# Performance work log

Measured on AMD Instinct MI355X. Metric: run time of the kernel, lower is better.

## Reference

```python
import jax, jax.numpy as jnp
import numpy as np

C = 512
H_HEADS = 8
HEAD_DIM = C // H_HEADS


def setup_inputs() -> dict:
    key = jax.random.key(0)
    ks = jax.random.split(key, 6)
    B, Hs, Ws = 16, 32, 32
    x = jax.random.normal(ks[0], (B, C, Hs, Ws), dtype=jnp.float32)
    qkv_w = jax.random.normal(ks[1], (3 * C, C), dtype=jnp.float32) * 0.02
    proj_w = jax.random.normal(ks[2], (C, C), dtype=jnp.float32) * 0.02
    proj_b = jnp.zeros((C,), dtype=jnp.float32)
    ln_g = jnp.ones((C,), dtype=jnp.float32)
    ln_b = jnp.zeros((C,), dtype=jnp.float32)
    return {"x": x, "qkv_w": qkv_w, "proj_w": proj_w, "proj_b": proj_b,
            "ln_g": ln_g, "ln_b": ln_b}


def _layernorm(x, g, b, eps=1e-5):
    mu = jnp.mean(x, axis=-1, keepdims=True)
    var = jnp.var(x, axis=-1, keepdims=True)
    return (x - mu) * jax.lax.rsqrt(var + eps) * g + b


def reference(x, qkv_w, proj_w, proj_b, ln_g, ln_b):
    B, Cc, Hs, Ws = x.shape
    N = Hs * Ws
    # (B, N, C)
    x_flat = x.reshape(B, Cc, N).transpose(0, 2, 1)
    x_norm = _layernorm(x_flat, ln_g, ln_b)
    # qkv: torch Linear y = x @ W^T
    qkv = x_norm @ qkv_w.T  # (B, N, 3C)
    qkv = qkv.reshape(B, N, 3, H_HEADS, HEAD_DIM).transpose(2, 0, 3, 1, 4)
    q, k, v = qkv[0], qkv[1], qkv[2]  # (B, h, N, d)
    scale = HEAD_DIM ** -0.5
    attn = jnp.einsum('bhnd,bhmd->bhnm', q, k) * scale
    attn = jax.nn.softmax(attn, axis=-1)
    out = jnp.einsum('bhnm,bhmd->bhnd', attn, v)  # (B, h, N, d)
    out = out.transpose(0, 2, 1, 3).reshape(B, N, Cc)
    out = out @ proj_w.T + proj_b
    out = out + x_flat
    return out.transpose(0, 2, 1).reshape(B, Cc, Hs, Ws)
```

## Files before the change

### kernel.cpp

```cpp
#include <hip/hip_runtime.h>
#include <stdint.h>

typedef unsigned short u16;
typedef __attribute__((ext_vector_type(4))) float f32x4;
typedef __attribute__((ext_vector_type(8))) short s16x8;
typedef __attribute__((ext_vector_type(4))) unsigned short u16x4;
typedef __attribute__((ext_vector_type(8))) unsigned short u16x8;
typedef __attribute__((ext_vector_type(2))) unsigned int u32x2;

__device__ __forceinline__ u16 f2bf(float f) {
  union { float f; uint32_t u; } v; v.f = f;
  uint32_t r = (v.u + 0x7FFFu + ((v.u >> 16) & 1u)) >> 16;
  return (u16)r;
}

__device__ __forceinline__ void gload_lds16(const void* g, void* l) {
  __builtin_amdgcn_global_load_lds((const __attribute__((address_space(1))) uint32_t*)g,
                                   (__attribute__((address_space(3))) uint32_t*)l, 16, 0, 0);
}

__global__ __launch_bounds__(256) void cvt_kernel(const float* __restrict__ src,
                                                  u16* __restrict__ dst, int n) {
  const int i = (blockIdx.x * 256 + threadIdx.x) * 4;
  if (i < n) {
    f32x4 v = *(const f32x4*)(src + i);
    u16x4 p;
    p[0] = f2bf(v[0]); p[1] = f2bf(v[1]); p[2] = f2bf(v[2]); p[3] = f2bf(v[3]);
    *(u16x4*)(dst + i) = p;
  }
}

__global__ __launch_bounds__(256) void ln_kernel(const float* __restrict__ x,
                                                 const float* __restrict__ lng,
                                                 const float* __restrict__ lnb,
                                                 u16* __restrict__ xn) {
  __shared__ float xt[16][516];
  __shared__ float ps[16][16], pq[16][16];
  __shared__ float smu[16], srs[16];
  const int tid = threadIdx.x;
  const int tok0 = blockIdx.x << 4;
  const int b = tok0 >> 10;
  const int nb = tok0 & 1023;
  const float* xb = x + (size_t)b * 512 * 1024 + nb;
  {
    const int n4 = (tid & 3) * 4;
    const int cr = tid >> 2;
#pragma unroll
    for (int it = 0; it < 8; ++it) {
      const int c = it * 64 + cr;
      f32x4 v = *(const f32x4*)(xb + (size_t)c * 1024 + n4);
      xt[n4 + 0][c] = v[0]; xt[n4 + 1][c] = v[1];
      xt[n4 + 2][c] = v[2]; xt[n4 + 3][c] = v[3];
    }
  }
  __syncthreads();
  {
    const int n = tid & 15, part = tid >> 4;
    float s = 0.f, q = 0.f;
#pragma unroll
    for (int i = 0; i < 8; ++i) {
      f32x4 v = *(const f32x4*)&xt[n][part * 32 + i * 4];
#pragma unroll
      for (int j = 0; j < 4; ++j) { s += v[j]; q += v[j] * v[j]; }
    }
    ps[part][n] = s; pq[part][n] = q;
  }
  __syncthreads();
  if (tid < 16) {
    float s = 0.f, q = 0.f;
#pragma unroll
    for (int p = 0; p < 16; ++p) { s += ps[p][tid]; q += pq[p][tid]; }
    const float mu = s * (1.f / 512.f);
    const float var = q * (1.f / 512.f) - mu * mu;
    smu[tid] = mu; srs[tid] = rsqrtf(var + 1e-5f);
  }
  __syncthreads();
  {
    const int n = tid >> 4, sub = tid & 15;
    const float mu = smu[n], rs = srs[n];
    u16* dst = xn + (size_t)(tok0 + n) * 512;
#pragma unroll
    for (int i = 0; i < 4; ++i) {
      const int c = (sub + 16 * i) * 8;
      f32x4 v0 = *(const f32x4*)&xt[n][c];
      f32x4 v1 = *(const f32x4*)&xt[n][c + 4];
      f32x4 g0 = *(const f32x4*)(lng + c);
      f32x4 g1 = *(const f32x4*)(lng + c + 4);
      f32x4 b0 = *(const f32x4*)(lnb + c);
      f32x4 b1 = *(const f32x4*)(lnb + c + 4);
      u16x8 pk;
#pragma unroll
      for (int j = 0; j < 4; ++j) {
        pk[j]     = f2bf((v0[j] - mu) * rs * g0[j] + b0[j]);
        pk[4 + j] = f2bf((v1[j] - mu) * rs * g1[j] + b1[j]);
      }
      *(u16x8*)(dst + c) = pk;
    }
  }
}

template <int EPI>
__global__ __launch_bounds__(256) void gemm_bt(const u16* __restrict__ A,
                                               const u16* __restrict__ Bw,
                                               void* __restrict__ Cout,
                                               const float* __restrict__ bias,
                                               const float* __restrict__ resid,
                                               int M, int N, int K,
                                               long bsz, long csz, long rsz) {
  __shared__ u16 Al[128 * 32];
  __shared__ u16 Bl[128 * 32];
  const int tid = threadIdx.x;
  const int w = tid >> 6, lane = tid & 63;
  const int lg = lane >> 4, l15 = lane & 15;
  const int wr = w >> 1, wc = w & 1;
  const int m0 = blockIdx.x * 128, n0 = blockIdx.y * 128;
  const int z = blockIdx.z;
  const u16* Bz = Bw + (size_t)z * bsz;
  const float* Rz = (EPI == 1) ? resid + (size_t)z * rsz : nullptr;

  f32x4 acc[4][4];
#pragma unroll
  for (int i = 0; i < 4; ++i)
#pragma unroll
    for (int j = 0; j < 4; ++j) acc[i][j] = (f32x4){0.f, 0.f, 0.f, 0.f};

  const int sr = lane >> 2, sch = (lane & 3) * 8;
  for (int k0 = 0; k0 < K; k0 += 32) {
    __syncthreads();
#pragma unroll
    for (int i = 0; i < 2; ++i) {
      gload_lds16(A + (size_t)(m0 + w * 32 + i * 16 + sr) * K + k0 + sch,
                  &Al[(w * 32 + i * 16) * 32]);
      gload_lds16(Bz + (size_t)(n0 + w * 32 + i * 16 + sr) * K + k0 + sch,
                  &Bl[(w * 32 + i * 16) * 32]);
    }
    __syncthreads();
    s16x8 af[4], bfr[4];
#pragma unroll
    for (int mi = 0; mi < 4; ++mi)
      af[mi] = *(const s16x8*)&Al[(wr * 64 + mi * 16 + l15) * 32 + lg * 8];
#pragma unroll
    for (int ni = 0; ni < 4; ++ni)
      bfr[ni] = *(const s16x8*)&Bl[(wc * 64 + ni * 16 + l15) * 32 + lg * 8];
#pragma unroll
    for (int mi = 0; mi < 4; ++mi)
#pragma unroll
      for (int ni = 0; ni < 4; ++ni)
        acc[mi][ni] = __builtin_amdgcn_mfma_f32_16x16x32_bf16(af[mi], bfr[ni], acc[mi][ni], 0, 0, 0);
  }

  if (EPI == 0) {
    u16* C = (u16*)Cout;
#pragma unroll
    for (int mi = 0; mi < 4; ++mi)
#pragma unroll
      for (int ni = 0; ni < 4; ++ni) {
        const int col = n0 + wc * 64 + ni * 16 + l15;
#pragma unroll
        for (int r = 0; r < 4; ++r) {
          const int row = m0 + wr * 64 + mi * 16 + lg * 4 + r;
          C[(size_t)row * N + col] = f2bf(acc[mi][ni][r]);
        }
      }
  } else {
    float* C = (float*)Cout + (size_t)z * csz;
#pragma unroll
    for (int mi = 0; mi < 4; ++mi)
#pragma unroll
      for (int ni = 0; ni < 4; ++ni) {
        const int col = n0 + wc * 64 + ni * 16 + l15;
#pragma unroll
        for (int r = 0; r < 4; ++r) {
          const int row = m0 + wr * 64 + mi * 16 + lg * 4 + r;
          C[(size_t)row * N + col] = acc[mi][ni][r] + bias[row] + Rz[(size_t)row * N + col];
        }
      }
  }
}

__global__ __launch_bounds__(256) void attn_kernel(const u16* __restrict__ qkv,
                                                   u16* __restrict__ ao) {
  __shared__ union {
    struct { u16 K[64 * 64]; uint32_t Vt[64 * 34]; } s;
    struct { float O[4 * 32 * 68]; float ls[4 * 32]; } e;
  } sm;
  const int tid = threadIdx.x;
  const int w = tid >> 6, lane = tid & 63;
  const int lg = lane >> 4, l15 = lane & 15;
  const int qb = blockIdx.x & 7, bh = blockIdx.x >> 3;
  const int b = bh >> 3, h = bh & 7;
  const size_t base = (size_t)b * 1024 * 1536;
  const int qtok0 = qb * 128 + w * 32;

  s16x8 qf[2][2];
#pragma unroll
  for (int s = 0; s < 2; ++s)
#pragma unroll
    for (int qg = 0; qg < 2; ++qg)
      qf[s][qg] = *(const s16x8*)(qkv + base + (size_t)(qtok0 + qg * 16 + l15) * 1536 +
                                  h * 64 + lg * 8 + 32 * s);

  f32x4 o[2][4];
#pragma unroll
  for (int qg = 0; qg < 2; ++qg)
#pragma unroll
    for (int db = 0; db < 4; ++db) o[qg][db] = (f32x4){0.f, 0.f, 0.f, 0.f};
  float mrun[2] = {-1e30f, -1e30f};
  float lrun[2] = {0.f, 0.f};
  const float CE = 0.125f * 1.44269504f;

  for (int k0 = 0; k0 < 1024; k0 += 64) {
    __syncthreads();
    {
      const int r = lane >> 3, ch = lane & 7;
#pragma unroll
      for (int i = 0; i < 2; ++i) {
        const int row = w * 16 + i * 8 + r;
        const u16* src = qkv + base + (size_t)(k0 + row) * 1536 + 512 + h * 64 +
                         ((ch ^ (row & 7)) * 8);
        gload_lds16(src, &sm.s.K[(w * 16 + i * 8) * 64]);
      }
    }
    {
      const int kk = tid & 63, dc = tid >> 6;
      const u16* v0p = qkv + base + (size_t)(k0 + kk) * 1536 + 1024 + h * 64 + dc * 8;
      u16x8 va = *(const u16x8*)v0p;
      u16x8 vc = *(const u16x8*)(v0p + 32);
      u16* vt16 = (u16*)sm.s.Vt;
      const int kp2 = kk >> 1, klo = kk & 1;
#pragma unroll
      for (int i = 0; i < 8; ++i) {
        const int d0 = dc * 8 + i;
        vt16[(d0 * 34 + kp2) * 2 + klo] = va[i];
        vt16[((d0 + 32) * 34 + kp2) * 2 + klo] = vc[i];
      }
    }
    __syncthreads();

    f32x4 st[4][2];
#pragma unroll
    for (int kg = 0; kg < 4; ++kg)
#pragma unroll
      for (int qg = 0; qg < 2; ++qg) st[kg][qg] = (f32x4){0.f, 0.f, 0.f, 0.f};
#pragma unroll
    for (int s = 0; s < 2; ++s)
#pragma unroll
      for (int kg = 0; kg < 4; ++kg) {
        const int row = kg * 16 + l15;
        s16x8 kf = *(const s16x8*)&sm.s.K[row * 64 + ((lg * 8 + 32 * s) ^ ((row & 7) << 3))];
#pragma unroll
        for (int qg = 0; qg < 2; ++qg)
          st[kg][qg] = __builtin_amdgcn_mfma_f32_16x16x32_bf16(kf, qf[s][qg], st[kg][qg], 0, 0, 0);
      }

    float pvv[2][16];
#pragma unroll
    for (int qg = 0; qg < 2; ++qg) {
      float tmax = -1e30f;
#pragma unroll
      for (int kg = 0; kg < 4; ++kg)
#pragma unroll
        for (int r = 0; r < 4; ++r) tmax = fmaxf(tmax, st[kg][qg][r]);
      tmax = fmaxf(tmax, __shfl_xor(tmax, 16));
      tmax = fmaxf(tmax, __shfl_xor(tmax, 32));
      const float mnew = fmaxf(mrun[qg], tmax);
      const float corr = exp2f((mrun[qg] - mnew) * CE);
      mrun[qg] = mnew;
      float tsum = 0.f;
#pragma unroll
      for (int kg = 0; kg < 4; ++kg)
#pragma unroll
        for (int r = 0; r < 4; ++r) {
          const float p = exp2f((st[kg][qg][r] - mnew) * CE);
          pvv[qg][kg * 4 + r] = p;
          tsum += p;
        }
      tsum += __shfl_xor(tsum, 16);
      tsum += __shfl_xor(tsum, 32);
      lrun[qg] = lrun[qg] * corr + tsum;
#pragma unroll
      for (int db = 0; db < 4; ++db)
#pragma unroll
        for (int r = 0; r < 4; ++r) o[qg][db][r] *= corr;
    }

    s16x8 pa[2][2];
#pragma unroll
    for (int qg = 0; qg < 2; ++qg)
#pragma unroll
      for (int kh = 0; kh < 2; ++kh) {
        s16x8 f;
#pragma unroll
        for (int j = 0; j < 4; ++j) {
          f[j]     = (short)f2bf(pvv[qg][(2 * kh) * 4 + j]);
          f[4 + j] = (short)f2bf(pvv[qg][(2 * kh + 1) * 4 + j]);
        }
        pa[qg][kh] = f;
      }

#pragma unroll
    for (int kh = 0; kh < 2; ++kh)
#pragma unroll
      for (int db = 0; db < 4; ++db) {
        const int d = db * 16 + l15;
        const uint32_t* vtp = sm.s.Vt + d * 34;
        u32x2 va = *(const u32x2*)(vtp + 16 * kh + 2 * lg);
        u32x2 vb = *(const u32x2*)(vtp + 16 * kh + 8 + 2 * lg);
        s16x8 vf;
        vf[0] = (short)(va[0] & 0xffff); vf[1] = (short)(va[0] >> 16);
        vf[2] = (short)(va[1] & 0xffff); vf[3] = (short)(va[1] >> 16);
        vf[4] = (short)(vb[0] & 0xffff); vf[5] = (short)(vb[0] >> 16);
        vf[6] = (short)(vb[1] & 0xffff); vf[7] = (short)(vb[1] >> 16);
#pragma unroll
        for (int qg = 0; qg < 2; ++qg)
          o[qg][db] = __builtin_amdgcn_mfma_f32_16x16x32_bf16(pa[qg][kh], vf, o[qg][db], 0, 0, 0);
      }
  }

  __syncthreads();
  float* Ow = sm.e.O + w * 32 * 68;
#pragma unroll
  for (int qg = 0; qg < 2; ++qg)
#pragma unroll
    for (int db = 0; db < 4; ++db)
#pragma unroll
      for (int r = 0; r < 4; ++r)
        Ow[(qg * 16 + lg * 4 + r) * 68 + db * 16 + l15] = o[qg][db][r];
  if (lane < 16) {
    sm.e.ls[w * 32 + lane] = lrun[0];
    sm.e.ls[w * 32 + 16 + lane] = lrun[1];
  }
  __syncthreads();
  {
    const int q = lane & 31, dh = lane >> 5;
    const float inv = 1.0f / sm.e.ls[w * 32 + q];
    u16* dst = ao + (size_t)(b * 1024 + qtok0 + q) * 512 + h * 64 + dh * 32;
#pragma unroll
    for (int i = 0; i < 4; ++i) {
      f32x4 v0 = *(const f32x4*)&Ow[q * 68 + dh * 32 + i * 8];
      f32x4 v1 = *(const f32x4*)&Ow[q * 68 + dh * 32 + i * 8 + 4];
      u16x8 pk;
#pragma unroll
      for (int j = 0; j < 4; ++j) { pk[j] = f2bf(v0[j] * inv); pk[4 + j] = f2bf(v1[j] * inv); }
      *(u16x8*)(dst + i * 8) = pk;
    }
  }
}

extern "C" void kernel_launch(void* const* d_in, const int* in_sizes, int n_in,
                              void* d_out, int out_size, void* d_ws, size_t ws_size,
                              hipStream_t stream) {
  const float* x      = (const float*)d_in[0];
  const float* qkv_w  = (const float*)d_in[1];
  const float* proj_w = (const float*)d_in[2];
  const float* proj_b = (const float*)d_in[3];
  const float* ln_g   = (const float*)d_in[4];
  const float* ln_b   = (const float*)d_in[5];
  float* out = (float*)d_out;

  char* ws = (char*)d_ws;
  u16* xn  = (u16*)ws;
  u16* qkv = (u16*)(ws + (size_t)16 * 1024 * 1024);
  u16* ao  = (u16*)(ws + (size_t)64 * 1024 * 1024);
  u16* qw  = (u16*)(ws + (size_t)80 * 1024 * 1024);
  u16* pw  = qw + 1536 * 512;

  cvt_kernel<<<768, 256, 0, stream>>>(qkv_w, qw, 1536 * 512);
  cvt_kernel<<<256, 256, 0, stream>>>(proj_w, pw, 512 * 512);
  ln_kernel<<<1024, 256, 0, stream>>>(x, ln_g, ln_b, xn);
  gemm_bt<0><<<dim3(128, 12, 1), 256, 0, stream>>>(xn, qw, qkv, nullptr, nullptr,
                                                   16384, 1536, 512, 0, 0, 0);
  attn_kernel<<<1024, 256, 0, stream>>>(qkv, ao);
  gemm_bt<1><<<dim3(4, 8, 16), 256, 0, stream>>>(pw, ao, out, proj_b, x,
                                                 512, 1024, 512,
                                                 (long)1024 * 512, (long)512 * 1024,
                                                 (long)512 * 1024);
}
```

Baseline: 258.6 us.

## Write V pre-transposed from QKV GEMM and double-buffer K/V in attention

The QKV GEMM epilogue now writes Q and K to a 1024-wide buffer and scatters V directly into a per-head transposed, pre-permuted layout. The attention kernel can then load both K and V with async global-to-LDS copies into double buffers, prefetching the next tile during compute and dropping one barrier per iteration. The old scalar LDS transpose of V goes away. Scalar bf16 rounding is replaced by the packed v_cvt_pk_bf16_f32 instruction, the softmax max and sum reductions use tree form, and occupancy is hinted via launch bounds. The V epilogue does scattered 8-byte stores, and the LDS footprint doubles.

```diff
diff --git a/kernel.cpp b/kernel.cpp
--- a/kernel.cpp
+++ b/kernel.cpp
@@ -6,12 +6,18 @@
 typedef __attribute__((ext_vector_type(8))) short s16x8;
 typedef __attribute__((ext_vector_type(4))) unsigned short u16x4;
 typedef __attribute__((ext_vector_type(8))) unsigned short u16x8;
-typedef __attribute__((ext_vector_type(2))) unsigned int u32x2;
+typedef __attribute__((ext_vector_type(4))) unsigned int u32x4;
 
 __device__ __forceinline__ u16 f2bf(float f) {
   union { float f; uint32_t u; } v; v.f = f;
   uint32_t r = (v.u + 0x7FFFu + ((v.u >> 16) & 1u)) >> 16;
   return (u16)r;
+}
+
+__device__ __forceinline__ uint32_t cvtpk(float lo, float hi) {
+  uint32_t r;
+  asm("v_cvt_pk_bf16_f32 %0, %1, %2" : "=v"(r) : "v"(lo), "v"(hi));
+  return r;
 }
 
 __device__ __forceinline__ void gload_lds16(const void* g, void* l) {
@@ -88,13 +94,18 @@
       f32x4 g1 = *(const f32x4*)(lng + c + 4);
       f32x4 b0 = *(const f32x4*)(lnb + c);
       f32x4 b1 = *(const f32x4*)(lnb + c + 4);
-      u16x8 pk;
-#pragma unroll
-      for (int j = 0; j < 4; ++j) {
-        pk[j]     = f2bf((v0[j] - mu) * rs * g0[j] + b0[j]);
-        pk[4 + j] = f2bf((v1[j] - mu) * rs * g1[j] + b1[j]);
-      }
-      *(u16x8*)(dst + c) = pk;
+      union { u32x4 w; u16x8 v; } pk;
+      float r0 = (v0[0] - mu) * rs * g0[0] + b0[0];
+      float r1 = (v0[1] - mu) * rs * g0[1] + b0[1];
+      float r2 = (v0[2] - mu) * rs * g0[2] + b0[2];
+      float r3 = (v0[3] - mu) * rs * g0[3] + b0[3];
+      float r4 = (v1[0] - mu) * rs * g1[0] + b1[0];
+      float r5 = (v1[1] - mu) * rs * g1[1] + b1[1];
+      float r6 = (v1[2] - mu) * rs * g1[2] + b1[2];
+      float r7 = (v1[3] - mu) * rs * g1[3] + b1[3];
+      pk.w[0] = cvtpk(r0, r1); pk.w[1] = cvtpk(r2, r3);
+      pk.w[2] = cvtpk(r4, r5); pk.w[3] = cvtpk(r6, r7);
+      *(u16x8*)(dst + c) = pk.v;
     }
   }
 }
@@ -103,6 +114,7 @@
 __global__ __launch_bounds__(256) void gemm_bt(const u16* __restrict__ A,
                                                const u16* __restrict__ Bw,
                                                void* __restrict__ Cout,
+                                               u16* __restrict__ vt,
                                                const float* __restrict__ bias,
                                                const float* __restrict__ resid,
                                                int M, int N, int K,
@@ -151,17 +163,36 @@
 
   if (EPI == 0) {
     u16* C = (u16*)Cout;
-#pragma unroll
-    for (int mi = 0; mi < 4; ++mi)
-#pragma unroll
-      for (int ni = 0; ni < 4; ++ni) {
-        const int col = n0 + wc * 64 + ni * 16 + l15;
-#pragma unroll
-        for (int r = 0; r < 4; ++r) {
-          const int row = m0 + wr * 64 + mi * 16 + lg * 4 + r;
-          C[(size_t)row * N + col] = f2bf(acc[mi][ni][r]);
+    if (n0 < 1024) {
+#pragma unroll
+      for (int mi = 0; mi < 4; ++mi)
+#pragma unroll
+        for (int ni = 0; ni < 4; ++ni) {
+          const int col = n0 + wc * 64 + ni * 16 + l15;
+          const int row = m0 + wr * 64 + mi * 16 + lg * 4;
+          const uint32_t w0 = cvtpk(acc[mi][ni][0], acc[mi][ni][1]);
+          const uint32_t w1 = cvtpk(acc[mi][ni][2], acc[mi][ni][3]);
+          C[(size_t)(row + 0) * 1024 + col] = (u16)w0;
+          C[(size_t)(row + 1) * 1024 + col] = (u16)(w0 >> 16);
+          C[(size_t)(row + 2) * 1024 + col] = (u16)w1;
+          C[(size_t)(row + 3) * 1024 + col] = (u16)(w1 >> 16);
         }
-      }
+    } else {
+#pragma unroll
+      for (int mi = 0; mi < 4; ++mi)
+#pragma unroll
+        for (int ni = 0; ni < 4; ++ni) {
+          const int vcol = n0 - 1024 + wc * 64 + ni * 16 + l15;
+          const int hh = vcol >> 6, d = vcol & 63;
+          const int token = m0 + wr * 64 + mi * 16 + lg * 4;
+          const int b = token >> 10, g15 = (token >> 6) & 15;
+          const int p = 32 * (mi >> 1) + 8 * lg + 4 * (mi & 1);
+          union { uint32_t w[2]; u16x4 v; } pk;
+          pk.w[0] = cvtpk(acc[mi][ni][0], acc[mi][ni][1]);
+          pk.w[1] = cvtpk(acc[mi][ni][2], acc[mi][ni][3]);
+          *(u16x4*)&vt[(size_t)((b * 8 + hh) * 64 + d) * 1024 + g15 * 64 + p] = pk.v;
+        }
+    }
   } else {
     float* C = (float*)Cout + (size_t)z * csz;
 #pragma unroll
@@ -178,10 +209,11 @@
   }
 }
 
-__global__ __launch_bounds__(256) void attn_kernel(const u16* __restrict__ qkv,
-                                                   u16* __restrict__ ao) {
+__global__ __launch_bounds__(256, 4) void attn_kernel(const u16* __restrict__ qk,
+                                                      const u16* __restrict__ vt,
+                                                      u16* __restrict__ ao) {
   __shared__ union {
-    struct { u16 K[64 * 64]; uint32_t Vt[64 * 34]; } s;
+    struct { u16 K[2][64 * 64]; u16 V[2][64 * 64]; } s;
     struct { float O[4 * 32 * 68]; float ls[4 * 32]; } e;
   } sm;
   const int tid = threadIdx.x;
@@ -189,7 +221,8 @@
   const int lg = lane >> 4, l15 = lane & 15;
   const int qb = blockIdx.x & 7, bh = blockIdx.x >> 3;
   const int b = bh >> 3, h = bh & 7;
-  const size_t base = (size_t)b * 1024 * 1536;
+  const size_t qbase = (size_t)b * 1024 * 1024;
+  const size_t vbase = (size_t)bh * 64 * 1024;
   const int qtok0 = qb * 128 + w * 32;
 
   s16x8 qf[2][2];
@@ -197,7 +230,7 @@
   for (int s = 0; s < 2; ++s)
 #pragma unroll
     for (int qg = 0; qg < 2; ++qg)
-      qf[s][qg] = *(const s16x8*)(qkv + base + (size_t)(qtok0 + qg * 16 + l15) * 1536 +
+      qf[s][qg] = *(const s16x8*)(qk + qbase + (size_t)(qtok0 + qg * 16 + l15) * 1024 +
                                   h * 64 + lg * 8 + 32 * s);
 
   f32x4 o[2][4];
@@ -209,33 +242,24 @@
   float lrun[2] = {0.f, 0.f};
   const float CE = 0.125f * 1.44269504f;
 
-  for (int k0 = 0; k0 < 1024; k0 += 64) {
-    __syncthreads();
-    {
-      const int r = lane >> 3, ch = lane & 7;
-#pragma unroll
-      for (int i = 0; i < 2; ++i) {
-        const int row = w * 16 + i * 8 + r;
-        const u16* src = qkv + base + (size_t)(k0 + row) * 1536 + 512 + h * 64 +
-                         ((ch ^ (row & 7)) * 8);
-        gload_lds16(src, &sm.s.K[(w * 16 + i * 8) * 64]);
-      }
-    }
-    {
-      const int kk = tid & 63, dc = tid >> 6;
-      const u16* v0p = qkv + base + (size_t)(k0 + kk) * 1536 + 1024 + h * 64 + dc * 8;
-      u16x8 va = *(const u16x8*)v0p;
-      u16x8 vc = *(const u16x8*)(v0p + 32);
-      u16* vt16 = (u16*)sm.s.Vt;
-      const int kp2 = kk >> 1, klo = kk & 1;
-#pragma unroll
-      for (int i = 0; i < 8; ++i) {
-        const int d0 = dc * 8 + i;
-        vt16[(d0 * 34 + kp2) * 2 + klo] = va[i];
-        vt16[((d0 + 32) * 34 + kp2) * 2 + klo] = vc[i];
-      }
-    }
-    __syncthreads();
+  const int srr = lane >> 3, sch = lane & 7;
+  auto stage = [&](int buf, int k0) {
+#pragma unroll
+    for (int i = 0; i < 2; ++i) {
+      const int row = w * 16 + i * 8 + srr;
+      gload_lds16(qk + qbase + (size_t)(k0 + row) * 1024 + 512 + h * 64 +
+                      ((sch ^ (row & 7)) * 8),
+                  &sm.s.K[buf][(w * 16 + i * 8) * 64]);
+      gload_lds16(vt + vbase + (size_t)row * 1024 + k0 + ((sch ^ (row & 7)) * 8),
+                  &sm.s.V[buf][(w * 16 + i * 8) * 64]);
+    }
+  };
+
+  stage(0, 0);
+  __syncthreads();
+  int cur = 0;
+  for (int t = 0; t < 16; ++t) {
+    if (t < 15) stage(cur ^ 1, (t + 1) * 64);
 
     f32x4 st[4][2];
 #pragma unroll
@@ -247,34 +271,42 @@
 #pragma unroll
       for (int kg = 0; kg < 4; ++kg) {
         const int row = kg * 16 + l15;
-        s16x8 kf = *(const s16x8*)&sm.s.K[row * 64 + ((lg * 8 + 32 * s) ^ ((row & 7) << 3))];
+        s16x8 kf = *(const s16x8*)&sm.s.K[cur][row * 64 +
+                                              ((lg * 8 + 32 * s) ^ ((row & 7) << 3))];
 #pragma unroll
         for (int qg = 0; qg < 2; ++qg)
           st[kg][qg] = __builtin_amdgcn_mfma_f32_16x16x32_bf16(kf, qf[s][qg], st[kg][qg], 0, 0, 0);
       }
 
-    float pvv[2][16];
+    s16x8 pa[2][2];
 #pragma unroll
     for (int qg = 0; qg < 2; ++qg) {
-      float tmax = -1e30f;
-#pragma unroll
-      for (int kg = 0; kg < 4; ++kg)
-#pragma unroll
-        for (int r = 0; r < 4; ++r) tmax = fmaxf(tmax, st[kg][qg][r]);
+      float t8[8];
+#pragma unroll
+      for (int kg = 0; kg < 4; ++kg) {
+        t8[2 * kg]     = fmaxf(st[kg][qg][0], st[kg][qg][1]);
+        t8[2 * kg + 1] = fmaxf(st[kg][qg][2], st[kg][qg][3]);
+      }
+      float tmax = fmaxf(fmaxf(fmaxf(t8[0], t8[1]), fmaxf(t8[2], t8[3])),
+                         fmaxf(fmaxf(t8[4], t8[5]), fmaxf(t8[6], t8[7])));
       tmax = fmaxf(tmax, __shfl_xor(tmax, 16));
       tmax = fmaxf(tmax, __shfl_xor(tmax, 32));
       const float mnew = fmaxf(mrun[qg], tmax);
       const float corr = exp2f((mrun[qg] - mnew) * CE);
       mrun[qg] = mnew;
-      float tsum = 0.f;
-#pragma unroll
-      for (int kg = 0; kg < 4; ++kg)
-#pragma unroll
-        for (int r = 0; r < 4; ++r) {
-          const float p = exp2f((st[kg][qg][r] - mnew) * CE);
-          pvv[qg][kg * 4 + r] = p;
-          tsum += p;
-        }
+      float pv[16], s8[8];
+#pragma unroll
+      for (int kg = 0; kg < 4; ++kg) {
+        const float p0 = exp2f((st[kg][qg][0] - mnew) * CE);
+        const float p1 = exp2f((st[kg][qg][1] - mnew) * CE);
+        const float p2 = exp2f((st[kg][qg][2] - mnew) * CE);
+        const float p3 = exp2f((st[kg][qg][3] - mnew) * CE);
+        pv[kg * 4 + 0] = p0; pv[kg * 4 + 1] = p1;
+        pv[kg * 4 + 2] = p2; pv[kg * 4 + 3] = p3;
+        s8[2 * kg] = p0 + p1; s8[2 * kg + 1] = p2 + p3;
+      }
+      float tsum = (s8[0] + s8[1]) + (s8[2] + s8[3]) +
+                   ((s8[4] + s8[5]) + (s8[6] + s8[7]));
       tsum += __shfl_xor(tsum, 16);
       tsum += __shfl_xor(tsum, 32);
       lrun[qg] = lrun[qg] * corr + tsum;
@@ -282,42 +314,33 @@
       for (int db = 0; db < 4; ++db)
 #pragma unroll
         for (int r = 0; r < 4; ++r) o[qg][db][r] *= corr;
-    }
-
-    s16x8 pa[2][2];
-#pragma unroll
-    for (int qg = 0; qg < 2; ++qg)
 #pragma unroll
       for (int kh = 0; kh < 2; ++kh) {
-        s16x8 f;
-#pragma unroll
-        for (int j = 0; j < 4; ++j) {
-          f[j]     = (short)f2bf(pvv[qg][(2 * kh) * 4 + j]);
-          f[4 + j] = (short)f2bf(pvv[qg][(2 * kh + 1) * 4 + j]);
-        }
-        pa[qg][kh] = f;
-      }
+        union { u32x4 w; s16x8 v; } pk;
+        pk.w[0] = cvtpk(pv[8 * kh + 0], pv[8 * kh + 1]);
+        pk.w[1] = cvtpk(pv[8 * kh + 2], pv[8 * kh + 3]);
+        pk.w[2] = cvtpk(pv[8 * kh + 4], pv[8 * kh + 5]);
+        pk.w[3] = cvtpk(pv[8 * kh + 6], pv[8 * kh + 7]);
+        pa[qg][kh] = pk.v;
+      }
+    }
 
 #pragma unroll
     for (int kh = 0; kh < 2; ++kh)
 #pragma unroll
       for (int db = 0; db < 4; ++db) {
         const int d = db * 16 + l15;
-        const uint32_t* vtp = sm.s.Vt + d * 34;
-        u32x2 va = *(const u32x2*)(vtp + 16 * kh + 2 * lg);
-        u32x2 vb = *(const u32x2*)(vtp + 16 * kh + 8 + 2 * lg);
-        s16x8 vf;
-        vf[0] = (short)(va[0] & 0xffff); vf[1] = (short)(va[0] >> 16);
-        vf[2] = (short)(va[1] & 0xffff); vf[3] = (short)(va[1] >> 16);
-        vf[4] = (short)(vb[0] & 0xffff); vf[5] = (short)(vb[0] >> 16);
-        vf[6] = (short)(vb[1] & 0xffff); vf[7] = (short)(vb[1] >> 16);
+        s16x8 vf = *(const s16x8*)&sm.s.V[cur][d * 64 +
+                                               ((kh * 32 + lg * 8) ^ ((d & 7) << 3))];
 #pragma unroll
         for (int qg = 0; qg < 2; ++qg)
           o[qg][db] = __builtin_amdgcn_mfma_f32_16x16x32_bf16(pa[qg][kh], vf, o[qg][db], 0, 0, 0);
       }
-  }
-
-  __syncthreads();
+
+    __syncthreads();
+    cur ^= 1;
+  }
+
   float* Ow = sm.e.O + w * 32 * 68;
 #pragma unroll
   for (int qg = 0; qg < 2; ++qg)
@@ -339,10 +362,12 @@
     for (int i = 0; i < 4; ++i) {
       f32x4 v0 = *(const f32x4*)&Ow[q * 68 + dh * 32 + i * 8];
       f32x4 v1 = *(const f32x4*)&Ow[q * 68 + dh * 32 + i * 8 + 4];
-      u16x8 pk;
-#pragma unroll
-      for (int j = 0; j < 4; ++j) { pk[j] = f2bf(v0[j] * inv); pk[4 + j] = f2bf(v1[j] * inv); }
-      *(u16x8*)(dst + i * 8) = pk;
+      union { u32x4 w; u16x8 v; } pk;
+      pk.w[0] = cvtpk(v0[0] * inv, v0[1] * inv);
+      pk.w[1] = cvtpk(v0[2] * inv, v0[3] * inv);
+      pk.w[2] = cvtpk(v1[0] * inv, v1[1] * inv);
+      pk.w[3] = cvtpk(v1[2] * inv, v1[3] * inv);
+      *(u16x8*)(dst + i * 8) = pk.v;
     }
   }
 }
@@ -360,7 +385,8 @@
 
   char* ws = (char*)d_ws;
   u16* xn  = (u16*)ws;
-  u16* qkv = (u16*)(ws + (size_t)16 * 1024 * 1024);
+  u16* qk  = (u16*)(ws + (size_t)16 * 1024 * 1024);
+  u16* vt  = (u16*)(ws + (size_t)48 * 1024 * 1024);
   u16* ao  = (u16*)(ws + (size_t)64 * 1024 * 1024);
   u16* qw  = (u16*)(ws + (size_t)80 * 1024 * 1024);
   u16* pw  = qw + 1536 * 512;
@@ -368,10 +394,10 @@
   cvt_kernel<<<768, 256, 0, stream>>>(qkv_w, qw, 1536 * 512);
   cvt_kernel<<<256, 256, 0, stream>>>(proj_w, pw, 512 * 512);
   ln_kernel<<<1024, 256, 0, stream>>>(x, ln_g, ln_b, xn);
-  gemm_bt<0><<<dim3(128, 12, 1), 256, 0, stream>>>(xn, qw, qkv, nullptr, nullptr,
-                                                   16384, 1536, 512, 0, 0, 0);
-  attn_kernel<<<1024, 256, 0, stream>>>(qkv, ao);
-  gemm_bt<1><<<dim3(4, 8, 16), 256, 0, stream>>>(pw, ao, out, proj_b, x,
+  gemm_bt<0><<<dim3(128, 12, 1), 256, 0, stream>>>(xn, qw, qk, vt, nullptr, nullptr,
+                                                   16384, 1024, 512, 0, 0, 0);
+  attn_kernel<<<1024, 256, 0, stream>>>(qk, vt, ao);
+  gemm_bt<1><<<dim3(4, 8, 16), 256, 0, stream>>>(pw, ao, out, nullptr, proj_b, x,
                                                  512, 1024, 512,
                                                  (long)1024 * 512, (long)512 * 1024,
                                                  (long)512 * 1024);
```

Measured after the change: 260.0 us. No clear change (+0.5%).
